# Optimization experiments

Measured on AMD Instinct MI355X. Metric: run time of the kernel, lower is better.

The kernel has to match this reference:

```python
import jax, jax.numpy as jnp
import numpy as np

H = 8           # num_heads
TANH_CLIP = 10.0


def setup_inputs() -> dict:
    key = jax.random.key(0)
    ks = jax.random.split(key, 7)
    B, N, D = 512, 1000, 128
    embeddings = jax.random.normal(ks[0], (B, N, D), dtype=jnp.float32)
    context_feat = jax.random.normal(ks[1], (B, 2 * D), dtype=jnp.float32)
    W_node = jax.random.normal(ks[2], (D, 3 * D), dtype=jnp.float32) / np.sqrt(D)
    W_fixed = jax.random.normal(ks[3], (D, D), dtype=jnp.float32) / np.sqrt(D)
    W_step = jax.random.normal(ks[4], (2 * D, D), dtype=jnp.float32) / np.sqrt(2 * D)
    W_out = jax.random.normal(ks[5], (D, D), dtype=jnp.float32) / np.sqrt(D)
    # action_mask: True = feasible node; ensure at least one feasible per row
    action_mask = jax.random.uniform(ks[6], (B, N)) > 0.3
    action_mask = action_mask.at[:, 0].set(True)
    return {"embeddings": embeddings, "context_feat": context_feat,
            "W_node": W_node, "W_fixed": W_fixed, "W_step": W_step,
            "W_out": W_out, "action_mask": action_mask}


def reference(embeddings, context_feat, W_node, W_fixed, W_step, W_out, action_mask):
    B, N, D = embeddings.shape
    dk = D // H
    # --- _precompute ---
    graph_context = (embeddings.mean(axis=1) @ W_fixed)[:, None, :]      # [B,1,D]
    proj = embeddings @ W_node                                            # [B,N,3D]
    gk, gv, logit_k = jnp.split(proj, 3, axis=-1)                         # each [B,N,D]
    to_heads = lambda x: x.reshape(B, N, H, dk).transpose(2, 0, 1, 3)     # [H,B,N,dk]
    K, V = to_heads(gk), to_heads(gv)
    # --- _get_log_p: query (num_steps = 1) ---
    q = graph_context + (context_feat @ W_step)[:, None, :]               # [B,1,D]
    Q = q.reshape(B, 1, H, dk).transpose(2, 0, 1, 3)                      # [H,B,1,dk]
    mask = ~action_mask                                                    # [B,N], True = infeasible
    # --- glimpse attention (mask_inner) ---
    compat = jnp.einsum('hbqd,hbnd->hbqn', Q, K) / jnp.sqrt(jnp.asarray(dk, Q.dtype))
    compat = jnp.where(mask[None, :, None, :], -jnp.inf, compat)
    attn = jax.nn.softmax(compat, axis=-1)                                 # [H,B,1,N]
    heads = jnp.einsum('hbqn,hbnd->hbqd', attn, V)                         # [H,B,1,dk]
    glimpse = heads.transpose(1, 2, 0, 3).reshape(B, 1, D) @ W_out         # [B,1,D]
    # --- tanh-clipped single-head logits ---
    logits = jnp.einsum('bqd,bnd->bqn', glimpse, logit_k) / jnp.sqrt(jnp.asarray(D, glimpse.dtype))
    logits = jnp.tanh(logits) * TANH_CLIP
    logits = jnp.where(mask[:, None, :], -jnp.inf, logits)                 # [B,1,N]
    return logits
```

## Files before the change

### kernel.cpp

```cpp
#include <hip/hip_runtime.h>
#include <math.h>

#define BB 512
#define NN 1000
#define DD 128
#define HH 8
#define TILE 125

#define WS_AFOLD 4096

__device__ __forceinline__ bool mask_feasible(const void* mask, int flag, int idx) {
    if (flag == 1) return ((const int*)mask)[idx] != 0;
    if (flag == 2) return ((const float*)mask)[idx] != 0.0f;
    return ((const unsigned char*)mask)[idx] != 0;
}

__device__ __forceinline__ void gload_lds16(const float4* g, float4* l) {
    __builtin_amdgcn_global_load_lds(
        (const __attribute__((address_space(1))) void*)g,
        (__attribute__((address_space(3))) void*)l,
        16, 0, 0);
}

__global__ void k0_detect(const unsigned int* __restrict__ m, int* __restrict__ flag) {
    int t = threadIdx.x;
    unsigned int w = m[t];
    unsigned long long bi = __ballot(w <= 1u);
    unsigned long long bf = __ballot(w == 0u || w == 0x3F800000u);
    if (t == 0) {
        int f = 0;
        if (bi == ~0ull) f = 1;
        else if (bf == ~0ull) f = 2;
        *flag = f;
    }
}

__global__ __launch_bounds__(512) void kA_meanfold(
    const float* __restrict__ emb, const float* __restrict__ ctx,
    const float* __restrict__ W_fixed, const float* __restrict__ W_step,
    const float* __restrict__ W_node, float* __restrict__ Afold) {
    int b = blockIdx.x, t = threadIdx.x;
    __shared__ float4 red[512];
    __shared__ float mean_s[DD], cld[2 * DD], qlds[DD];
    int q4 = t & 31, j = t >> 5;
    const float4* e4 = (const float4*)(emb + (size_t)b * NN * DD);
    float4 acc = {0.f, 0.f, 0.f, 0.f};
    for (int n = j; n < NN; n += 16) {
        float4 v = e4[n * 32 + q4];
        acc.x += v.x; acc.y += v.y; acc.z += v.z; acc.w += v.w;
    }
    red[t] = acc;
    __syncthreads();
    for (int s = 8; s >= 1; s >>= 1) {
        if (j < s) {
            float4 o = red[t + s * 32], m = red[t];
            m.x += o.x; m.y += o.y; m.z += o.z; m.w += o.w;
            red[t] = m;
        }
        __syncthreads();
    }
    if (t < 32) {
        float4 m = red[t];
        const float inv = 1.0f / (float)NN;
        ((float4*)mean_s)[t] = make_float4(m.x * inv, m.y * inv, m.z * inv, m.w * inv);
    }
    if (t < 256) cld[t] = ctx[b * 2 * DD + t];
    __syncthreads();
    if (t < 128) {
        float a = 0.f;
        for (int c = 0; c < DD; ++c)     a += mean_s[c] * W_fixed[c * DD + t];
        for (int c = 0; c < 2 * DD; ++c) a += cld[c] * W_step[c * DD + t];
        qlds[t] = a;
    }
    __syncthreads();
    if (t < 128) {
        const float* wrow = W_node + (size_t)t * 3 * DD;
        float* A2 = Afold + (size_t)b * 1024;
        for (int h = 0; h < HH; ++h) {
            float a = 0.f;
#pragma unroll
            for (int d0 = 0; d0 < 16; ++d0) a += wrow[h * 16 + d0] * qlds[h * 16 + d0];
            A2[t * 8 + h] = 0.25f * a;
        }
    }
}

__global__ __launch_bounds__(256) void kB_flash(
    const float* __restrict__ emb, const float* __restrict__ Afold,
    const void* __restrict__ mask, const int* __restrict__ flagp,
    const float* __restrict__ W_node, const float* __restrict__ W_out,
    float* __restrict__ out) {
    int b = blockIdx.x, t = threadIdx.x;
    int flag = *flagp;
    int wave = t >> 6, lane = t & 63;
    int hq = (t >> 7) * 4;
    int n = t & 127;
    int c4 = t & 31, jr = t >> 5;

    __shared__ float4 tile4[128][32];
    __shared__ float cbuf[128][8];
    __shared__ float wemb_s[8][128];
    __shared__ float small[3 * DD];
    __shared__ float zl[HH];

    int hqs = __builtin_amdgcn_readfirstlane(hq);
    const float* AbW = Afold + (size_t)b * 1024 + hqs;

    float4 wacc[8];
#pragma unroll
    for (int h = 0; h < HH; ++h) wacc[h] = make_float4(0.f, 0.f, 0.f, 0.f);
    float zrun = 0.f;

    const float4* embB4 = (const float4*)(emb + (size_t)b * NN * DD);
    const int mbase = b * NN;
    float4* tl = (float4*)tile4;

    for (int tile = 0; tile < 8; ++tile) {
        int n0 = tile * TILE;
        for (int i = wave; i < 63; i += 4) {
            int p0 = i * 64;
            int p = p0 + lane;
            int r = p >> 5; if (r > 124) r = 124;
            int c = (p & 31) ^ (r & 31);
            gload_lds16(embB4 + (size_t)(n0 + r) * 32 + c, &tl[p0]);
        }
        __syncthreads();
        if (n < TILE) {
            int sw = n & 31;
            float4 s = make_float4(0.f, 0.f, 0.f, 0.f);
#pragma unroll 8
            for (int k = 0; k < 32; ++k) {
                float4 e = tile4[n][k ^ sw];
                const float* ak = AbW + k * 32;
                s.x += e.x * ak[0] + e.y * ak[8]  + e.z * ak[16] + e.w * ak[24];
                s.y += e.x * ak[1] + e.y * ak[9]  + e.z * ak[17] + e.w * ak[25];
                s.z += e.x * ak[2] + e.y * ak[10] + e.z * ak[18] + e.w * ak[26];
                s.w += e.x * ak[3] + e.y * ak[11] + e.z * ak[19] + e.w * ak[27];
            }
            bool feas = mask_feasible(mask, flag, mbase + n0 + n);
            float4 p = make_float4(0.f, 0.f, 0.f, 0.f);
            if (feas) {
                p.x = __expf(s.x); p.y = __expf(s.y);
                p.z = __expf(s.z); p.w = __expf(s.w);
            }
            *(float4*)&cbuf[n][hq] = p;
        }
        __syncthreads();
        if (t < 64) {
            int h = t & 7, seg = t >> 3;
            float z = 0.f;
            for (int nn = seg; nn < TILE; nn += 8) z += cbuf[nn][h];
            z += __shfl_xor(z, 8);
            z += __shfl_xor(z, 16);
            z += __shfl_xor(z, 32);
            if (t < 8) zrun += z;
        }
        for (int nn = jr; nn < TILE; nn += 8) {
            float4 e = tile4[nn][c4 ^ (nn & 31)];
            float4 pA = *(const float4*)&cbuf[nn][0];
            float4 pB = *(const float4*)&cbuf[nn][4];
            wacc[0].x += pA.x * e.x; wacc[0].y += pA.x * e.y; wacc[0].z += pA.x * e.z; wacc[0].w += pA.x * e.w;
            wacc[1].x += pA.y * e.x; wacc[1].y += pA.y * e.y; wacc[1].z += pA.y * e.z; wacc[1].w += pA.y * e.w;
            wacc[2].x += pA.z * e.x; wacc[2].y += pA.z * e.y; wacc[2].z += pA.z * e.z; wacc[2].w += pA.z * e.w;
            wacc[3].x += pA.w * e.x; wacc[3].y += pA.w * e.y; wacc[3].z += pA.w * e.z; wacc[3].w += pA.w * e.w;
            wacc[4].x += pB.x * e.x; wacc[4].y += pB.x * e.y; wacc[4].z += pB.x * e.z; wacc[4].w += pB.x * e.w;
            wacc[5].x += pB.y * e.x; wacc[5].y += pB.y * e.y; wacc[5].z += pB.y * e.z; wacc[5].w += pB.y * e.w;
            wacc[6].x += pB.z * e.x; wacc[6].y += pB.z * e.y; wacc[6].z += pB.z * e.z; wacc[6].w += pB.z * e.w;
            wacc[7].x += pB.w * e.x; wacc[7].y += pB.w * e.y; wacc[7].z += pB.w * e.z; wacc[7].w += pB.w * e.w;
        }
        __syncthreads();
    }
    if (t < 8) zl[t] = zrun;
    {
        float4* red = (float4*)&tile4[0][0];
#pragma unroll
        for (int h = 0; h < HH; ++h) red[(jr * 32 + c4) * 8 + h] = wacc[h];
        __syncthreads();
        int cc = t >> 3, hh = t & 7;
        float4 s = make_float4(0.f, 0.f, 0.f, 0.f);
#pragma unroll
        for (int jj = 0; jj < 8; ++jj) {
            float4 v = red[(jj * 32 + cc) * 8 + hh];
            s.x += v.x; s.y += v.y; s.z += v.z; s.w += v.w;
        }
        float inv = 1.0f / zl[hh];
        s.x *= inv; s.y *= inv; s.z *= inv; s.w *= inv;
        *(float4*)&wemb_s[hh][cc * 4] = s;
    }
    __syncthreads();
    if (t < 128) {
        int h = t >> 4;
        float a = 0.f;
        for (int c = 0; c < DD; ++c) a += wemb_s[h][c] * W_node[(size_t)c * 384 + 128 + t];
        small[t] = a;
    }
    __syncthreads();
    if (t < 128) {
        float g = 0.f;
        for (int k = 0; k < DD; ++k) g += small[k] * W_out[k * DD + t];
        small[128 + t] = g;
    }
    __syncthreads();
    if (t < 128) {
        float a3 = 0.f;
        const float* wr = W_node + (size_t)t * 384 + 256;
        for (int d = 0; d < DD; ++d) a3 += wr[d] * small[128 + d];
        small[256 + t] = a3;
    }
    __syncthreads();
    const float4* g2v = (const float4*)&small[256];
    for (int r = t; r < NN; r += 256) {
        const float4* row = embB4 + (size_t)r * 32;
        float acc = 0.f;
#pragma unroll 8
        for (int k = 0; k < 32; ++k) {
            float4 e = row[k], g = g2v[k];
            acc += e.x * g.x + e.y * g.y + e.z * g.z + e.w * g.w;
        }
        bool feas = mask_feasible(mask, flag, mbase + r);
        out[(size_t)mbase + r] = feas ? (10.0f * tanhf(acc * 0.08838834764831845f)) : -1.0e30f;
    }
}

extern "C" void kernel_launch(void* const* d_in, const int* in_sizes, int n_in,
                              void* d_out, int out_size, void* d_ws, size_t ws_size,
                              hipStream_t stream) {
    (void)in_sizes; (void)n_in; (void)out_size; (void)ws_size;
    const float* emb     = (const float*)d_in[0];
    const float* ctx     = (const float*)d_in[1];
    const float* W_node  = (const float*)d_in[2];
    const float* W_fixed = (const float*)d_in[3];
    const float* W_step  = (const float*)d_in[4];
    const float* W_out   = (const float*)d_in[5];
    const void*  mask    = d_in[6];
    float* out = (float*)d_out;

    char* ws = (char*)d_ws;
    int*   flag  = (int*)(ws + 0);
    float* Afold = (float*)(ws + WS_AFOLD);

    k0_detect<<<1, 64, 0, stream>>>((const unsigned int*)mask, flag);
    kA_meanfold<<<BB, 512, 0, stream>>>(emb, ctx, W_fixed, W_step, W_node, Afold);
    kB_flash<<<BB, 256, 0, stream>>>(emb, Afold, mask, flag, W_node, W_out, out);
}
```

Before: 166.4 us.

## Double-buffer embedding tiles with async LDS loads and shrink tile to 64 rows

The attention kernel now streams embeddings in 64-row tiles into two LDS buffers, issuing the global-to-LDS load for the next tile before computing the current one. This overlaps memory fetch with compute and removes the barrier that waited on each load. Each wave now computes two heads per row over 64 rows, so all 256 threads do score work instead of the previous layout where some threads had no row. It also reuses the staging buffer for the later reductions to cut LDS use. The cost is twice as many tile iterations and barriers.

After: 185.2 us. +11.2%, slower.

```diff
diff --git a/kernel.cpp b/kernel.cpp
--- a/kernel.cpp
+++ b/kernel.cpp
@@ -5,7 +5,8 @@
 #define NN 1000
 #define DD 128
 #define HH 8
-#define TILE 125
+#define TILE 64
+#define NT 16
 
 #define WS_AFOLD 4096
 
@@ -93,14 +94,12 @@
     int b = blockIdx.x, t = threadIdx.x;
     int flag = *flagp;
     int wave = t >> 6, lane = t & 63;
-    int hq = (t >> 7) * 4;
-    int n = t & 127;
+    int hq = wave * 2;
+    int n = lane;
     int c4 = t & 31, jr = t >> 5;
 
-    __shared__ float4 tile4[128][32];
-    __shared__ float cbuf[128][8];
-    __shared__ float wemb_s[8][128];
-    __shared__ float small[3 * DD];
+    __shared__ float4 buf2[2][TILE * 32];
+    __shared__ float cbufs[TILE * 8];
     __shared__ float zl[HH];
 
     int hqs = __builtin_amdgcn_readfirstlane(hq);
@@ -113,52 +112,60 @@
 
     const float4* embB4 = (const float4*)(emb + (size_t)b * NN * DD);
     const int mbase = b * NN;
-    float4* tl = (float4*)tile4;
-
-    for (int tile = 0; tile < 8; ++tile) {
-        int n0 = tile * TILE;
-        for (int i = wave; i < 63; i += 4) {
+
+    auto stage = [&](int dst, int n0, int rows) {
+        int nchunks = (rows * 32) >> 6;
+        float4* base = buf2[dst];
+        for (int i = wave; i < nchunks; i += 4) {
             int p0 = i * 64;
             int p = p0 + lane;
-            int r = p >> 5; if (r > 124) r = 124;
+            int r = p >> 5;
             int c = (p & 31) ^ (r & 31);
-            gload_lds16(embB4 + (size_t)(n0 + r) * 32 + c, &tl[p0]);
-        }
-        __syncthreads();
-        if (n < TILE) {
+            gload_lds16(embB4 + (size_t)(n0 + r) * 32 + c, base + p0);
+        }
+    };
+
+    stage(0, 0, TILE);
+    __syncthreads();
+    int cur = 0;
+
+    for (int tile = 0; tile < NT; ++tile) {
+        int n0 = tile * TILE;
+        int rows = (NN - n0 < TILE) ? (NN - n0) : TILE;
+        if (tile < NT - 1) {
+            int n1 = n0 + TILE;
+            int rows1 = (NN - n1 < TILE) ? (NN - n1) : TILE;
+            stage(cur ^ 1, n1, rows1);
+        }
+        const float4* tb = buf2[cur];
+        if (n < rows) {
             int sw = n & 31;
-            float4 s = make_float4(0.f, 0.f, 0.f, 0.f);
+            float sx = 0.f, sy = 0.f;
 #pragma unroll 8
             for (int k = 0; k < 32; ++k) {
-                float4 e = tile4[n][k ^ sw];
+                float4 e = tb[n * 32 + (k ^ sw)];
                 const float* ak = AbW + k * 32;
-                s.x += e.x * ak[0] + e.y * ak[8]  + e.z * ak[16] + e.w * ak[24];
-                s.y += e.x * ak[1] + e.y * ak[9]  + e.z * ak[17] + e.w * ak[25];
-                s.z += e.x * ak[2] + e.y * ak[10] + e.z * ak[18] + e.w * ak[26];
-                s.w += e.x * ak[3] + e.y * ak[11] + e.z * ak[19] + e.w * ak[27];
+                sx += e.x * ak[0] + e.y * ak[8] + e.z * ak[16] + e.w * ak[24];
+                sy += e.x * ak[1] + e.y * ak[9] + e.z * ak[17] + e.w * ak[25];
             }
             bool feas = mask_feasible(mask, flag, mbase + n0 + n);
-            float4 p = make_float4(0.f, 0.f, 0.f, 0.f);
-            if (feas) {
-                p.x = __expf(s.x); p.y = __expf(s.y);
-                p.z = __expf(s.z); p.w = __expf(s.w);
-            }
-            *(float4*)&cbuf[n][hq] = p;
+            cbufs[n * 8 + hq]     = feas ? __expf(sx) : 0.f;
+            cbufs[n * 8 + hq + 1] = feas ? __expf(sy) : 0.f;
         }
         __syncthreads();
         if (t < 64) {
             int h = t & 7, seg = t >> 3;
             float z = 0.f;
-            for (int nn = seg; nn < TILE; nn += 8) z += cbuf[nn][h];
+            for (int nn = seg; nn < rows; nn += 8) z += cbufs[nn * 8 + h];
             z += __shfl_xor(z, 8);
             z += __shfl_xor(z, 16);
             z += __shfl_xor(z, 32);
             if (t < 8) zrun += z;
         }
-        for (int nn = jr; nn < TILE; nn += 8) {
-            float4 e = tile4[nn][c4 ^ (nn & 31)];
-            float4 pA = *(const float4*)&cbuf[nn][0];
-            float4 pB = *(const float4*)&cbuf[nn][4];
+        for (int nn = jr; nn < rows; nn += 8) {
+            float4 e = tb[nn * 32 + (c4 ^ (nn & 31))];
+            float4 pA = *(const float4*)&cbufs[nn * 8];
+            float4 pB = *(const float4*)&cbufs[nn * 8 + 4];
             wacc[0].x += pA.x * e.x; wacc[0].y += pA.x * e.y; wacc[0].z += pA.x * e.z; wacc[0].w += pA.x * e.w;
             wacc[1].x += pA.y * e.x; wacc[1].y += pA.y * e.y; wacc[1].z += pA.y * e.z; wacc[1].w += pA.y * e.w;
             wacc[2].x += pA.z * e.x; wacc[2].y += pA.z * e.y; wacc[2].z += pA.z * e.z; wacc[2].w += pA.z * e.w;
@@ -169,10 +176,12 @@
             wacc[7].x += pB.w * e.x; wacc[7].y += pB.w * e.y; wacc[7].z += pB.w * e.z; wacc[7].w += pB.w * e.w;
         }
         __syncthreads();
+        cur ^= 1;
     }
     if (t < 8) zl[t] = zrun;
+    float4 wsum;
     {
-        float4* red = (float4*)&tile4[0][0];
+        float4* red = (float4*)buf2;
 #pragma unroll
         for (int h = 0; h < HH; ++h) red[(jr * 32 + c4) * 8 + h] = wacc[h];
         __syncthreads();
@@ -184,14 +193,20 @@
             s.x += v.x; s.y += v.y; s.z += v.z; s.w += v.w;
         }
         float inv = 1.0f / zl[hh];
-        s.x *= inv; s.y *= inv; s.z *= inv; s.w *= inv;
-        *(float4*)&wemb_s[hh][cc * 4] = s;
+        wsum = make_float4(s.x * inv, s.y * inv, s.z * inv, s.w * inv);
+    }
+    __syncthreads();
+    float* wemb_s = (float*)buf2;
+    float* small  = (float*)buf2 + 1024;
+    {
+        int cc = t >> 3, hh = t & 7;
+        *(float4*)&wemb_s[hh * 128 + cc * 4] = wsum;
     }
     __syncthreads();
     if (t < 128) {
         int h = t >> 4;
         float a = 0.f;
-        for (int c = 0; c < DD; ++c) a += wemb_s[h][c] * W_node[(size_t)c * 384 + 128 + t];
+        for (int c = 0; c < DD; ++c) a += wemb_s[h * 128 + c] * W_node[(size_t)c * 384 + 128 + t];
         small[t] = a;
     }
     __syncthreads();
```
